# Optimization experiments

Hardware: AMD Instinct MI355X
Metric: run time of the kernel (lower is better)

Reference implementation:

```python
import jax, jax.numpy as jnp
import numpy as np

E_DIM = 64
N_EMBED = 8192

def setup_inputs() -> dict:
    key = jax.random.key(0)
    k1, k2 = jax.random.split(key)
    x = jax.random.normal(k1, (16, E_DIM, 32, 32), dtype=jnp.float32)   # [B, e_dim, H, W]
    embed = jax.random.normal(k2, (E_DIM, N_EMBED), dtype=jnp.float32)  # codebook [e_dim, n_embed]
    return {"x": x, "embed": embed}

def reference(x, embed):
    e_dim, n_embed = embed.shape
    # NCHW -> NHWC
    xp = jnp.transpose(x, (0, 2, 3, 1))              # [B, H, W, e_dim]
    flat = xp.reshape(-1, e_dim)                     # [N, e_dim]
    # squared-distance expansion: ||f||^2 - 2 f.E + ||e||^2  -> [N, n_embed]
    distance = (jnp.sum(flat * flat, axis=1, keepdims=True)
                - 2.0 * flat @ embed
                + jnp.sum(embed * embed, axis=0, keepdims=True))
    embed_idx = jnp.argmax(-distance, axis=1)        # [N] nearest code ids
    embed_idx = embed_idx.reshape(xp.shape[:-1])     # [B, H, W]
    # gather codes: embedding table is embed.T -> [n_embed, e_dim]
    quantize = jnp.take(embed.T, embed_idx, axis=0)  # [B, H, W, e_dim]
    return quantize
```

## Files before the change

kernel.cpp:

```cpp
#include <hip/hip_runtime.h>


typedef __attribute__((ext_vector_type(8))) __bf16 bf16x8;
typedef __attribute__((ext_vector_type(4))) float f32x4;
typedef unsigned int u32;
typedef unsigned long long u64;

union frag_cast { f32x4 f; bf16x8 b; };
__device__ __forceinline__ bf16x8 as_bf16x8(f32x4 v) { frag_cast u; u.f = v; return u.b; }

#define N_ROWS  16384
#define E_DIM   64
#define N_EMBED 8192
#define NCHUNK  16
#define COLS_PER_BLOCK (N_EMBED / NCHUNK)
#define N_ST (COLS_PER_BLOCK / 64)
#define ROWS_PER_BLOCK 512
#define N_ROWBLK (N_ROWS / ROWS_PER_BLOCK)
#define NT 8
#define MARGIN_THR 2e-3f

#define WS_AH   0u
#define WS_AL   (2u << 20)
#define WS_B    (4u << 20)
#define WS_ET   (6u << 20)
#define WS_BIAS (8u << 20)
#define WS_CNT  (WS_BIAS + (32u << 10))
#define WS_PB1  (WS_CNT + (4u << 10))
#define WS_PI1  (WS_PB1 + (1u << 20))
#define WS_PB2  (WS_PI1 + (1u << 20))

__device__ __forceinline__ u32 f32_key(float s) {
    u32 u = __float_as_uint(s);
    return (u & 0x80000000u) ? ~u : (u | 0x80000000u);
}

__device__ __forceinline__ void async16(const void* g, void* l) {
    __builtin_amdgcn_global_load_lds(
        (const __attribute__((address_space(1))) void*)g,
        (__attribute__((address_space(3))) void*)l, 16, 0, 0);
}

__global__ __launch_bounds__(256) void prep(
        const float* __restrict__ x, const float* __restrict__ embed, char* ws) {
    __shared__ float tile[64][65];
    __bf16* Ah = (__bf16*)(ws + WS_AH);
    __bf16* Al = (__bf16*)(ws + WS_AL);
    float*  eT = (float*)(ws + WS_ET);
    float*  bias = (float*)(ws + WS_BIAS);
    const int t = threadIdx.x;
    const int blk = blockIdx.x;

    if (blk < 256) {
        const int b = blk >> 4, p0 = (blk & 15) * 64;
        {
            const int c = t >> 2, seg = (t & 3) * 16;
            const float* src = x + b * 65536 + c * 1024 + p0 + seg;
#pragma unroll
            for (int i = 0; i < 16; ++i) tile[c][seg + i] = src[i];
        }
        __syncthreads();
        const int p = t >> 2, cq = (t & 3) * 16;
        const long row = b * 1024 + p0 + p;
        bf16x8 vh0, vh1, vl0, vl1;
#pragma unroll
        for (int i = 0; i < 16; ++i) {
            float f = tile[cq + i][p];
            __bf16 h = (__bf16)f;
            __bf16 l = (__bf16)(f - (float)h);
            if (i < 8) { vh0[i] = h; vl0[i] = l; }
            else       { vh1[i - 8] = h; vl1[i - 8] = l; }
        }
        *(bf16x8*)(Ah + row * 64 + cq) = vh0;
        *(bf16x8*)(Ah + row * 64 + cq + 8) = vh1;
        *(bf16x8*)(Al + row * 64 + cq) = vl0;
        *(bf16x8*)(Al + row * 64 + cq + 8) = vl1;
    } else {
        const int g = blk - 256;
        const int jbase = g * 64;
        char* Bg = ws + WS_B + (size_t)g * 16384;
        {
            const int c = t >> 2, seg = (t & 3) * 16;
            const float* src = embed + c * N_EMBED + jbase + seg;
#pragma unroll
            for (int i = 0; i < 16; ++i) tile[c][seg + i] = src[i];
        }
        __syncthreads();
        if (t < 64) {
            float s = 0.f;
#pragma unroll
            for (int c = 0; c < 64; ++c) { float v = tile[c][t]; s = fmaf(v, v, s); }
            bias[jbase + t] = -0.5f * s;
        }
        const int jl = t >> 2, cq = (t & 3) * 16;
        bf16x8 vh0, vh1, vl0, vl1;
#pragma unroll
        for (int i = 0; i < 16; ++i) {
            float f = tile[cq + i][jl];
            eT[(long)(jbase + jl) * 64 + cq + i] = f;
            __bf16 h = (__bf16)f;
            __bf16 l = (__bf16)(f - (float)h);
            if (i < 8) { vh0[i] = h; vl0[i] = l; }
            else       { vh1[i - 8] = h; vl1[i - 8] = l; }
        }
        const int k0 = (cq >> 3), sw = jl & 7;
        __bf16* hi = (__bf16*)Bg + jl * 64;
        __bf16* lo = (__bf16*)(Bg + 8192) + jl * 64;
        *(bf16x8*)(hi + ((k0 ^ sw) * 8))       = vh0;
        *(bf16x8*)(hi + (((k0 + 1) ^ sw) * 8)) = vh1;
        *(bf16x8*)(lo + ((k0 ^ sw) * 8))       = vl0;
        *(bf16x8*)(lo + (((k0 + 1) ^ sw) * 8)) = vl1;
    }
}

__global__ __launch_bounds__(256, 2) void qdist(const char* __restrict__ ws_c, char* __restrict__ ws) {
    __shared__ __align__(16) char smem[2][16384];
    const __bf16* Ah = (const __bf16*)(ws_c + WS_AH);
    const __bf16* Al = (const __bf16*)(ws_c + WS_AL);
    const char* Bws = ws_c + WS_B;
    const float* biasg = (const float*)(ws_c + WS_BIAS);
    float* pb1 = (float*)(ws + WS_PB1);
    int*   pi1 = (int*)(ws + WS_PI1);
    float* pb2 = (float*)(ws + WS_PB2);

    const int t = threadIdx.x;
    const int wv = t >> 6, lane = t & 63, ln = lane & 15, q = lane >> 4;
    const int rb = blockIdx.x >> 4, chunk = blockIdx.x & 15;
    const int row0 = rb * ROWS_PER_BLOCK;
    const int col0 = chunk * COLS_PER_BLOCK;
    const int g0 = col0 >> 6;

    f32x4 pfh[NT][2], pfl[NT][2];
#pragma unroll
    for (int nt = 0; nt < NT; ++nt) {
        long row = row0 + wv * 128 + nt * 16 + ln;
        long base = row * 64 + q * 8;
        pfh[nt][0] = *(const f32x4*)(Ah + base);
        pfh[nt][1] = *(const f32x4*)(Ah + base + 32);
        pfl[nt][0] = *(const f32x4*)(Al + base);
        pfl[nt][1] = *(const f32x4*)(Al + base + 32);
    }
    asm volatile("" :
        "+v"(pfh[0][0]), "+v"(pfh[0][1]), "+v"(pfh[1][0]), "+v"(pfh[1][1]),
        "+v"(pfh[2][0]), "+v"(pfh[2][1]), "+v"(pfh[3][0]), "+v"(pfh[3][1]),
        "+v"(pfh[4][0]), "+v"(pfh[4][1]), "+v"(pfh[5][0]), "+v"(pfh[5][1]),
        "+v"(pfh[6][0]), "+v"(pfh[6][1]), "+v"(pfh[7][0]), "+v"(pfh[7][1]));
    asm volatile("" :
        "+v"(pfl[0][0]), "+v"(pfl[0][1]), "+v"(pfl[1][0]), "+v"(pfl[1][1]),
        "+v"(pfl[2][0]), "+v"(pfl[2][1]), "+v"(pfl[3][0]), "+v"(pfl[3][1]),
        "+v"(pfl[4][0]), "+v"(pfl[4][1]), "+v"(pfl[5][0]), "+v"(pfl[5][1]),
        "+v"(pfl[6][0]), "+v"(pfl[6][1]), "+v"(pfl[7][0]), "+v"(pfl[7][1]));

    float b1[NT], b2[NT]; int iq[NT];
#pragma unroll
    for (int k = 0; k < NT; ++k) { b1[k] = -3.4e38f; b2[k] = -3.4e38f; iq[k] = 0; }

    const int s7 = ln & 7;
    const int rdbase = ln * 128 + ((q ^ s7) << 4);

    auto issue = [&](int st) {
        const char* src = Bws + (size_t)(g0 + st) * 16384;
        char* dst = smem[st & 1];
#pragma unroll
        for (int s = 0; s < 4; ++s)
            async16(src + s * 4096 + wv * 1024 + lane * 16,
                    dst + s * 4096 + wv * 1024);
    };

    issue(0);
    for (int st = 0; st < N_ST; ++st) {
        __syncthreads();
        if (st + 1 < N_ST) issue(st + 1);
        const char* buf = smem[st & 1];
        __builtin_amdgcn_s_setprio(1);
#pragma unroll
        for (int ct = 0; ct < 4; ++ct) {
            const int boff = ct * 2048 + rdbase;
            bf16x8 ah0 = *(const bf16x8*)(buf + boff);
            bf16x8 ah1 = *(const bf16x8*)(buf + (boff ^ 64));
            bf16x8 al0 = *(const bf16x8*)(buf + 8192 + boff);
            bf16x8 al1 = *(const bf16x8*)(buf + 8192 + (boff ^ 64));
            const int cbase = col0 + st * 64 + ct * 16;
            f32x4 bv = *(const f32x4*)(biasg + cbase + q * 4);
            const int jq = cbase + q * 4;
#pragma unroll
            for (int nt = 0; nt < NT; ++nt) {
                f32x4 acc = __builtin_amdgcn_mfma_f32_16x16x32_bf16(al0, as_bf16x8(pfh[nt][0]), bv, 0, 0, 0);
                acc = __builtin_amdgcn_mfma_f32_16x16x32_bf16(al1, as_bf16x8(pfh[nt][1]), acc, 0, 0, 0);
                acc = __builtin_amdgcn_mfma_f32_16x16x32_bf16(ah0, as_bf16x8(pfl[nt][0]), acc, 0, 0, 0);
                acc = __builtin_amdgcn_mfma_f32_16x16x32_bf16(ah1, as_bf16x8(pfl[nt][1]), acc, 0, 0, 0);
                acc = __builtin_amdgcn_mfma_f32_16x16x32_bf16(ah0, as_bf16x8(pfh[nt][0]), acc, 0, 0, 0);
                acc = __builtin_amdgcn_mfma_f32_16x16x32_bf16(ah1, as_bf16x8(pfh[nt][1]), acc, 0, 0, 0);
                float mx = fmaxf(fmaxf(acc[0], acc[1]), fmaxf(acc[2], acc[3]));
                b2[nt] = fmaxf(b2[nt], fminf(b1[nt], mx));
                bool gt = mx > b1[nt];
                b1[nt] = fmaxf(b1[nt], mx);
                iq[nt] = gt ? jq : iq[nt];
            }
        }
        __builtin_amdgcn_s_setprio(0);
    }

#pragma unroll
    for (int m = 16; m < 64; m <<= 1) {
#pragma unroll
        for (int nt = 0; nt < NT; ++nt) {
            float o1 = __shfl_xor(b1[nt], m);
            int   oi = __shfl_xor(iq[nt], m);
            float o2 = __shfl_xor(b2[nt], m);
            b2[nt] = fmaxf(fmaxf(fminf(b1[nt], o1), o2), b2[nt]);
            bool take = (o1 > b1[nt]) || (o1 == b1[nt] && oi < iq[nt]);
            if (take) { b1[nt] = o1; iq[nt] = oi; }
        }
    }
    if (q == 0) {
#pragma unroll
        for (int nt = 0; nt < NT; ++nt) {
            int pixel = row0 + wv * 128 + nt * 16 + ln;
            int o = chunk * N_ROWS + pixel;
            pb1[o] = b1[nt];
            pi1[o] = iq[nt];
            pb2[o] = b2[nt];
        }
    }
}

__global__ __launch_bounds__(256) void reduce_rows(const float* __restrict__ x, char* ws,
                                                   float* __restrict__ out) {
    __shared__ float fl[64][65];
    const float* pb1 = (const float*)(ws + WS_PB1);
    const int*   pi1 = (const int*)(ws + WS_PI1);
    const float* pb2 = (const float*)(ws + WS_PB2);
    const float* eT = (const float*)(ws + WS_ET);
    const float* bias = (const float*)(ws + WS_BIAS);
    const int t = threadIdx.x;
    const int lane = t & 63, wv = t >> 6;
    const int row = (blockIdx.x * 256 + t) >> 2;
    const int sub = t & 3;
    const int rl = (row & 1023) & 63;

    {
        const int b = blockIdx.x >> 4;
        const int p0 = (blockIdx.x * 64) & 1023;
        const int c = t >> 2, seg = sub * 16;
        const float* src = x + b * 65536 + c * 1024 + p0 + seg;
#pragma unroll
        for (int i = 0; i < 16; ++i) fl[c][seg + i] = src[i];
    }
    __syncthreads();

    float m1 = -3.4e38f, m2 = -3.4e38f; int mi = 0;
#pragma unroll
    for (int k = 0; k < 4; ++k) {
        const int ch = sub * 4 + k;
        float o1 = pb1[ch * N_ROWS + row];
        int   oi = pi1[ch * N_ROWS + row];
        float o2 = pb2[ch * N_ROWS + row];
        m2 = fmaxf(fmaxf(fminf(m1, o1), o2), m2);
        if (o1 > m1 || (o1 == m1 && oi < mi)) { m1 = o1; mi = oi; }
    }
#pragma unroll
    for (int m = 1; m < 4; m <<= 1) {
        float o1 = __shfl_xor(m1, m);
        int   oi = __shfl_xor(mi, m);
        float o2 = __shfl_xor(m2, m);
        m2 = fmaxf(fmaxf(fminf(m1, o1), o2), m2);
        bool take = (o1 > m1) || (o1 == m1 && oi < mi);
        if (take) { m1 = o1; mi = oi; }
    }

    const bool flagged = (m1 - m2 < MARGIN_THR);
    if (!flagged) {
        const int j = mi + sub;
        const f32x4* ecd = (const f32x4*)(eT + (size_t)j * 64);
        float s = bias[j];
#pragma unroll
        for (int v = 0; v < 16; ++v) {
            f32x4 ev = ecd[v];
            s = fmaf(fl[v * 4 + 0][rl], ev[0], s);
            s = fmaf(fl[v * 4 + 1][rl], ev[1], s);
            s = fmaf(fl[v * 4 + 2][rl], ev[2], s);
            s = fmaf(fl[v * 4 + 3][rl], ev[3], s);
        }
        float best = s; int bj = j;
#pragma unroll
        for (int m = 1; m < 4; m <<= 1) {
            float os = __shfl_xor(best, m);
            int   oj = __shfl_xor(bj, m);
            bool take = (os > best) || (os == best && oj < bj);
            if (take) { best = os; bj = oj; }
        }
        const f32x4* src = (const f32x4*)(eT + (size_t)bj * 64);
        f32x4* dst = (f32x4*)(out + (size_t)row * 64);
#pragma unroll
        for (int v = 0; v < 4; ++v) dst[v * 4 + sub] = src[v * 4 + sub];
    }

    u64 bal = __ballot(flagged);
    const int wrow0 = blockIdx.x * 64 + wv * 16;
    while (bal) {
        const int b = __ffsll(bal) - 1;
        const int rw = b >> 2;
        bal &= ~(0xFull << (rw * 4));
        const int r = wrow0 + rw;
        const int rlr = wv * 16 + rw;
        const float rb1 = __shfl(m1, rw * 4);
        const float cutoff = rb1 - 2.0f * MARGIN_THR;

        float xr[64];
#pragma unroll
        for (int c = 0; c < 64; ++c) xr[c] = fl[c][rlr];

        u64 bestk = 0ull;
        for (int ch = 0; ch < NCHUNK; ++ch) {
            if (pb1[ch * N_ROWS + r] < cutoff) continue;
#pragma unroll
            for (int k = 0; k < 8; ++k) {
                const int j = ch * 512 + lane * 8 + k;
                const f32x4* ecd = (const f32x4*)(eT + (size_t)j * 64);
                f32x4 a0 = {0.f, 0.f, 0.f, 0.f}, a1 = a0, a2 = a0, a3 = a0;
#pragma unroll
                for (int v = 0; v < 4; ++v) {
                    f32x4 e0 = ecd[v * 4 + 0], e1 = ecd[v * 4 + 1];
                    f32x4 e2 = ecd[v * 4 + 2], e3 = ecd[v * 4 + 3];
#pragma unroll
                    for (int kk = 0; kk < 4; ++kk) {
                        a0[kk] = fmaf(xr[v * 16 + kk],      e0[kk], a0[kk]);
                        a1[kk] = fmaf(xr[v * 16 + 4 + kk],  e1[kk], a1[kk]);
                        a2[kk] = fmaf(xr[v * 16 + 8 + kk],  e2[kk], a2[kk]);
                        a3[kk] = fmaf(xr[v * 16 + 12 + kk], e3[kk], a3[kk]);
                    }
                }
                f32x4 a01 = a0 + a1, a23 = a2 + a3;
                f32x4 as = a01 + a23;
                float s = bias[j] + ((as[0] + as[1]) + (as[2] + as[3]));
                u64 key = ((u64)f32_key(s) << 32) | (u32)(~(u32)j);
                bestk = (key > bestk) ? key : bestk;
            }
        }
#pragma unroll
        for (int m = 1; m < 64; m <<= 1) {
            u64 o = __shfl_xor(bestk, m);
            bestk = (o > bestk) ? o : bestk;
        }
        const int idx = (int)(~(u32)(bestk & 0xffffffffull));
        out[(size_t)r * 64 + lane] = eT[(size_t)idx * 64 + lane];
    }
}

extern "C" void kernel_launch(void* const* d_in, const int* in_sizes, int n_in,
                              void* d_out, int out_size, void* d_ws, size_t ws_size,
                              hipStream_t stream) {
    const float* x     = (const float*)d_in[0];
    const float* embed = (const float*)d_in[1];
    float* out = (float*)d_out;
    char* ws = (char*)d_ws;

    prep<<<384, 256, 0, stream>>>(x, embed, ws);
    qdist<<<N_ROWBLK * NCHUNK, 256, 0, stream>>>(ws, ws);
    reduce_rows<<<256, 256, 0, stream>>>(x, ws, out);
}
```

Baseline: 131.9 us.

## Split codebook into 32 chunks and pack runner-up score with index

Doubles the number of codebook column chunks so the distance kernel launches twice as many blocks, each covering 256 codes. To offset the larger partial-result traffic, the runner-up score (rounded up to fp16) and the 16-bit index are packed into one 32-bit word, cutting per-chunk partial storage from three arrays to two. The reduction and fallback rescoring kernels are adjusted to read 32 chunks. Risks include extra reduction reads and a coarser runner-up value that can flag more rows for exact rescoring.

```diff
diff --git a/kernel.cpp b/kernel.cpp
--- a/kernel.cpp
+++ b/kernel.cpp
@@ -4,6 +4,7 @@
 typedef __attribute__((ext_vector_type(8))) __bf16 bf16x8;
 typedef __attribute__((ext_vector_type(4))) float f32x4;
 typedef unsigned int u32;
+typedef unsigned short u16;
 typedef unsigned long long u64;
 
 union frag_cast { f32x4 f; bf16x8 b; };
@@ -12,7 +13,7 @@
 #define N_ROWS  16384
 #define E_DIM   64
 #define N_EMBED 8192
-#define NCHUNK  16
+#define NCHUNK  32
 #define COLS_PER_BLOCK (N_EMBED / NCHUNK)
 #define N_ST (COLS_PER_BLOCK / 64)
 #define ROWS_PER_BLOCK 512
@@ -25,10 +26,19 @@
 #define WS_B    (4u << 20)
 #define WS_ET   (6u << 20)
 #define WS_BIAS (8u << 20)
-#define WS_CNT  (WS_BIAS + (32u << 10))
-#define WS_PB1  (WS_CNT + (4u << 10))
-#define WS_PI1  (WS_PB1 + (1u << 20))
-#define WS_PB2  (WS_PI1 + (1u << 20))
+#define WS_PB1  (WS_BIAS + (64u << 10))
+#define WS_PX   (WS_PB1 + (2u << 20))
+
+union h16 { _Float16 h; u16 s; };
+
+__device__ __forceinline__ u32 pack_b2_iq(float b2, int iq) {
+    h16 u; u.h = (_Float16)b2;
+    if ((float)u.h < b2) u.s += (b2 >= 0.f) ? 1 : (u16)0xFFFF;
+    return ((u32)u.s << 16) | (u32)(iq & 0xffff);
+}
+__device__ __forceinline__ float unpack_b2(u32 p) {
+    h16 u; u.s = (u16)(p >> 16); return (float)u.h;
+}
 
 __device__ __forceinline__ u32 f32_key(float s) {
     u32 u = __float_as_uint(s);
@@ -120,12 +130,11 @@
     const char* Bws = ws_c + WS_B;
     const float* biasg = (const float*)(ws_c + WS_BIAS);
     float* pb1 = (float*)(ws + WS_PB1);
-    int*   pi1 = (int*)(ws + WS_PI1);
-    float* pb2 = (float*)(ws + WS_PB2);
+    u32*   px  = (u32*)(ws + WS_PX);
 
     const int t = threadIdx.x;
     const int wv = t >> 6, lane = t & 63, ln = lane & 15, q = lane >> 4;
-    const int rb = blockIdx.x >> 4, chunk = blockIdx.x & 15;
+    const int rb = blockIdx.x >> 5, chunk = blockIdx.x & 31;
     const int row0 = rb * ROWS_PER_BLOCK;
     const int col0 = chunk * COLS_PER_BLOCK;
     const int g0 = col0 >> 6;
@@ -219,8 +228,7 @@
             int pixel = row0 + wv * 128 + nt * 16 + ln;
             int o = chunk * N_ROWS + pixel;
             pb1[o] = b1[nt];
-            pi1[o] = iq[nt];
-            pb2[o] = b2[nt];
+            px[o]  = pack_b2_iq(b2[nt], iq[nt]);
         }
     }
 }
@@ -229,8 +237,7 @@
                                                    float* __restrict__ out) {
     __shared__ float fl[64][65];
     const float* pb1 = (const float*)(ws + WS_PB1);
-    const int*   pi1 = (const int*)(ws + WS_PI1);
-    const float* pb2 = (const float*)(ws + WS_PB2);
+    const u32*   px  = (const u32*)(ws + WS_PX);
     const float* eT = (const float*)(ws + WS_ET);
     const float* bias = (const float*)(ws + WS_BIAS);
     const int t = threadIdx.x;
@@ -251,11 +258,12 @@
 
     float m1 = -3.4e38f, m2 = -3.4e38f; int mi = 0;
 #pragma unroll
-    for (int k = 0; k < 4; ++k) {
-        const int ch = sub * 4 + k;
+    for (int k = 0; k < 8; ++k) {
+        const int ch = sub * 8 + k;
         float o1 = pb1[ch * N_ROWS + row];
-        int   oi = pi1[ch * N_ROWS + row];
-        float o2 = pb2[ch * N_ROWS + row];
+        u32   pk = px[ch * N_ROWS + row];
+        int   oi = (int)(pk & 0xffffu);
+        float o2 = unpack_b2(pk);
         m2 = fmaxf(fmaxf(fminf(m1, o1), o2), m2);
         if (o1 > m1 || (o1 == m1 && oi < mi)) { m1 = o1; mi = oi; }
     }
@@ -315,8 +323,8 @@
         for (int ch = 0; ch < NCHUNK; ++ch) {
             if (pb1[ch * N_ROWS + r] < cutoff) continue;
 #pragma unroll
-            for (int k = 0; k < 8; ++k) {
-                const int j = ch * 512 + lane * 8 + k;
+            for (int k = 0; k < 4; ++k) {
+                const int j = ch * 256 + lane * 4 + k;
                 const f32x4* ecd = (const f32x4*)(eT + (size_t)j * 64);
                 f32x4 a0 = {0.f, 0.f, 0.f, 0.f}, a1 = a0, a2 = a0, a3 = a0;
 #pragma unroll
```

Measured after the change: 136.9 us. +3.9%, slower.
